# Kernel optimization log

Hardware: AMD Instinct MI355X
Metric: run time of the kernel (lower is better)

Reference implementation:

```python
import jax, jax.numpy as jnp
import numpy as np

EPS = 1e-10
BETA_SCALE = 1.0
TEMP = 0.5


def setup_inputs() -> dict:
    key = jax.random.key(0)
    ks = jax.random.split(key, 8)
    D = 128
    return {
        "root_mu_min": jax.random.normal(ks[0], (1, 64, D), dtype=jnp.float32),
        "root_mu_max": jax.random.normal(ks[1], (1, 64, D), dtype=jnp.float32),
        "root_beta_min_raw": jax.random.normal(ks[2], (1, 64, D), dtype=jnp.float32),
        "root_beta_max_raw": jax.random.normal(ks[3], (1, 64, D), dtype=jnp.float32),
        "adj_logits0": jax.random.normal(ks[4], (512, 64), dtype=jnp.float32),
        "adj_logits1": jax.random.normal(ks[5], (2048, 512), dtype=jnp.float32),
        "u0": jax.random.uniform(ks[6], (1, 512, 64), dtype=jnp.float32),
        "u1": jax.random.uniform(ks[7], (1, 2048, 512), dtype=jnp.float32),
    }


def _gumbel_sigmoid_hard(logits, u):
    # gumbel noise from externally supplied uniforms, straight-through hard threshold
    g = -jnp.log(-jnp.log(u + EPS) + EPS)
    y_soft = jax.nn.sigmoid((logits + g) / TEMP)
    y_hard = (y_soft > 0.5).astype(y_soft.dtype)
    return y_hard - jax.lax.stop_gradient(y_soft) + y_soft


def _weighted_intersection(mu_min, mu_max, beta_min, beta_max, w):
    # w: (1, C, P); parent boxes: (1, P, D)
    wsum = jnp.sum(w, axis=2)[..., None] + EPS                      # (1, C, 1)
    b_min = jnp.einsum('bcp,bpd->bcd', w, beta_min) / wsum           # (1, C, D)
    b_max = jnp.einsum('bcp,bpd->bcd', w, beta_max) / wsum           # (1, C, D)
    logw = jnp.log(w + EPS)[..., None]                               # (1, C, P, 1)
    arg_min = logw + mu_min[:, None, :, :] / b_min[:, :, None, :]    # (1, C, P, D)
    mu_min_i = b_min * jax.nn.logsumexp(arg_min, axis=2)             # (1, C, D)
    arg_max = logw - mu_max[:, None, :, :] / b_max[:, :, None, :]    # (1, C, P, D)
    mu_max_i = -b_max * jax.nn.logsumexp(arg_max, axis=2)            # (1, C, D)
    return mu_min_i, mu_max_i, b_min, b_max


def reference(root_mu_min, root_mu_max, root_beta_min_raw, root_beta_max_raw,
              adj_logits0, adj_logits1, u0, u1):
    beta_min = jax.nn.sigmoid(root_beta_min_raw) * BETA_SCALE + 1e-6
    beta_max = jax.nn.sigmoid(root_beta_max_raw) * BETA_SCALE + 1e-6
    level = (root_mu_min, root_mu_max, beta_min, beta_max)
    outs = list(level)
    for logits, u in ((adj_logits0, u0), (adj_logits1, u1)):
        w = _gumbel_sigmoid_hard(logits[None], u)  # (1, C, P)
        level = _weighted_intersection(*level, w)
        outs.extend(level)
    return tuple(outs)
```

## Files before the change

kernel.cpp:

```cpp
#include <hip/hip_runtime.h>
#include <cmath>

#define DD 128
#define LOG2E 1.4426950408889634f

__device__ __forceinline__ float sigm(float x) { return 1.0f / (1.0f + __expf(-x)); }

__global__ __launch_bounds__(512, 4)
void k_lvl1(const float* __restrict__ mu_min0, const float* __restrict__ mu_max0,
            const float* __restrict__ braw_min, const float* __restrict__ braw_max,
            const float* __restrict__ adj0, const float* __restrict__ u0,
            float* __restrict__ out,
            float2* __restrict__ mu2_1, float2* __restrict__ bb2_1,
            float4* __restrict__ pmax) {
    __shared__ __align__(16) float wsh[64][4];
    __shared__ int npres[4];
    __shared__ float4 red[8][4][64];
    __shared__ float4 cmx[8][64];
    __shared__ float4 carrA[4][64], carrB[4][64];
    const int tid = threadIdx.x;
    const int w = tid >> 6, lane = tid & 63;
    const int c0 = blockIdx.x * 4;

    if (tid < 64) {
        int i = blockIdx.x * 64 + tid;
        out[i] = mu_min0[i];
        out[8192 + i] = mu_max0[i];
        out[16384 + i] = sigm(braw_min[i]) + 1e-6f;
        out[24576 + i] = sigm(braw_max[i]) + 1e-6f;
    }

    if (tid < 256) {
        int j = tid >> 6, p = tid & 63;
        int idx = (c0 + j) * 64 + p;
        float uu = u0[idx] + 1e-10f;
        float g = -__logf(-__logf(uu) + 1e-10f);
        bool pres = (adj0[idx] + g) > 0.0f;
        wsh[p][j] = pres ? 1.0f : 1e-10f;
        unsigned long long m = __ballot(pres);
        if ((tid & 63) == 0) npres[j] = (int)__popcll(m);
    }
    __syncthreads();

    const int p0 = w * 8;
    const int dbase = 2 * lane;

    float4 accB[4];
    #pragma unroll
    for (int j = 0; j < 4; ++j) accB[j] = make_float4(0.f, 0.f, 0.f, 0.f);
    float4 mrow[8];
    float cm_mn0 = -INFINITY, cm_mn1 = -INFINITY, cm_ng0 = -INFINITY, cm_ng1 = -INFINITY;
    #pragma unroll
    for (int z = 0; z < 8; ++z) {
        int p = p0 + z;
        float2 bmr = *(const float2*)(braw_min + p * DD + dbase);
        float2 bxr = *(const float2*)(braw_max + p * DD + dbase);
        float2 mnr = *(const float2*)(mu_min0 + p * DD + dbase);
        float2 mxr = *(const float2*)(mu_max0 + p * DD + dbase);
        float bm0 = sigm(bmr.x) + 1e-6f, bm1 = sigm(bmr.y) + 1e-6f;
        float bx0 = sigm(bxr.x) + 1e-6f, bx1 = sigm(bxr.y) + 1e-6f;
        mrow[z] = make_float4(mnr.x, mxr.x, mnr.y, mxr.y);
        cm_mn0 = fmaxf(cm_mn0, mnr.x); cm_mn1 = fmaxf(cm_mn1, mnr.y);
        cm_ng0 = fmaxf(cm_ng0, -mxr.x); cm_ng1 = fmaxf(cm_ng1, -mxr.y);
        float4 wv = *(const float4*)wsh[p];
        const float* wf = (const float*)&wv;
        #pragma unroll
        for (int j = 0; j < 4; ++j) {
            accB[j].x = fmaf(wf[j], bm0, accB[j].x);
            accB[j].y = fmaf(wf[j], bx0, accB[j].y);
            accB[j].z = fmaf(wf[j], bm1, accB[j].z);
            accB[j].w = fmaf(wf[j], bx1, accB[j].w);
        }
    }
    #pragma unroll
    for (int j = 0; j < 4; ++j) red[w][j][lane] = accB[j];
    cmx[w][lane] = make_float4(cm_mn0, cm_ng0, cm_mn1, cm_ng1);
    __syncthreads();

    float bmin0, bmax0, bmin1, bmax1, rmin0, rmin1, nrmax0, nrmax1, Mm0, Mm1, Mg0, Mg1;
    const int rj = tid >> 6;
    if (tid < 256) {
        float4 S = red[0][rj][lane];
        float4 M = cmx[0][lane];
        #pragma unroll
        for (int ww = 1; ww < 8; ++ww) {
            float4 t = red[ww][rj][lane];
            S.x += t.x; S.y += t.y; S.z += t.z; S.w += t.w;
            float4 m = cmx[ww][lane];
            M.x = fmaxf(M.x, m.x); M.y = fmaxf(M.y, m.y);
            M.z = fmaxf(M.z, m.z); M.w = fmaxf(M.w, m.w);
        }
        Mm0 = M.x; Mg0 = M.y; Mm1 = M.z; Mg1 = M.w;
        const float wsv = (float)npres[rj] + 1e-10f;
        bmin0 = S.x / wsv; bmax0 = S.y / wsv; bmin1 = S.z / wsv; bmax1 = S.w / wsv;
        rmin0 = 1.0f / fmaxf(bmin0, 1e-30f);
        rmin1 = 1.0f / fmaxf(bmin1, 1e-30f);
        nrmax0 = -1.0f / fmaxf(bmax0, 1e-30f);
        nrmax1 = -1.0f / fmaxf(bmax1, 1e-30f);
        float rm20 = rmin0 * LOG2E, rm21 = rmin1 * LOG2E;
        float nx20 = nrmax0 * LOG2E, nx21 = nrmax1 * LOG2E;
        carrA[rj][lane] = make_float4(rm20, rm21, nx20, nx21);
        carrB[rj][lane] = make_float4(-rm20 * Mm0, -rm21 * Mm1, nx20 * Mg0, nx21 * Mg1);
    }
    __syncthreads();

    float4 cA[4], cB[4];
    #pragma unroll
    for (int j = 0; j < 4; ++j) { cA[j] = carrA[j][lane]; cB[j] = carrB[j][lane]; }

    float4 accS[4];
    #pragma unroll
    for (int j = 0; j < 4; ++j) accS[j] = make_float4(0.f, 0.f, 0.f, 0.f);
    #pragma unroll
    for (int z = 0; z < 8; ++z) {
        float4 q = mrow[z];
        float4 wv = *(const float4*)wsh[p0 + z];
        const float* wf = (const float*)&wv;
        #pragma unroll
        for (int j = 0; j < 4; ++j) {
            accS[j].x = fmaf(wf[j], __builtin_amdgcn_exp2f(fmaf(q.x, cA[j].x, cB[j].x)), accS[j].x);
            accS[j].y = fmaf(wf[j], __builtin_amdgcn_exp2f(fmaf(q.y, cA[j].z, cB[j].z)), accS[j].y);
            accS[j].z = fmaf(wf[j], __builtin_amdgcn_exp2f(fmaf(q.z, cA[j].y, cB[j].y)), accS[j].z);
            accS[j].w = fmaf(wf[j], __builtin_amdgcn_exp2f(fmaf(q.w, cA[j].w, cB[j].w)), accS[j].w);
        }
    }
    #pragma unroll
    for (int j = 0; j < 4; ++j) red[w][j][lane] = accS[j];
    __syncthreads();

    if (tid < 256) {
        float4 S = red[0][rj][lane];
        #pragma unroll
        for (int ww = 1; ww < 8; ++ww) {
            float4 t = red[ww][rj][lane];
            S.x += t.x; S.y += t.y; S.z += t.z; S.w += t.w;
        }
        const float S10 = fmaxf(S.x, 1e-35f);
        const float S20 = fmaxf(S.y, 1e-35f);
        const float S11 = fmaxf(S.z, 1e-35f);
        const float S21 = fmaxf(S.w, 1e-35f);
        const int cc = c0 + rj;
        const int idx = cc * DD + 2 * lane;
        float v10 = bmin0 * fmaf(rmin0, Mm0, __logf(S10));
        float v11 = bmin1 * fmaf(rmin1, Mm1, __logf(S11));
        float v20 = -bmax0 * fmaf(-nrmax0, Mg0, __logf(S20));
        float v21 = -bmax1 * fmaf(-nrmax1, Mg1, __logf(S21));
        *(float2*)(out + 32768 + idx)  = make_float2(v10, v11);
        *(float2*)(out + 98304 + idx)  = make_float2(v20, v21);
        *(float2*)(out + 163840 + idx) = make_float2(bmin0, bmin1);
        *(float2*)(out + 229376 + idx) = make_float2(bmax0, bmax1);
        *(float4*)(mu2_1 + idx) = make_float4(v10, v20, v11, v21);
        *(float4*)(bb2_1 + idx) = make_float4(bmin0, bmax0, bmin1, bmax1);
        red[0][rj][lane] = make_float4(v10, -v20, v11, -v21);
    }
    __syncthreads();
    if (tid < 64) {
        float4 m = red[0][0][tid];
        #pragma unroll
        for (int jj = 1; jj < 4; ++jj) {
            float4 t = red[0][jj][tid];
            m.x = fmaxf(m.x, t.x); m.y = fmaxf(m.y, t.y);
            m.z = fmaxf(m.z, t.z); m.w = fmaxf(m.w, t.w);
        }
        pmax[blockIdx.x * 64 + tid] = m;
    }
}

__global__ __launch_bounds__(512, 4)
void k_level2d(const float* __restrict__ logits, const float* __restrict__ u,
               const float2* __restrict__ bb2, const float2* __restrict__ mu2,
               const float4* __restrict__ pmax,
               float* __restrict__ o_mu_min, float* __restrict__ o_mu_max,
               float* __restrict__ o_b_min, float* __restrict__ o_b_max) {
    constexpr int P = 512, TC = 4;
    __shared__ __align__(16) float wsh[P][TC];
    __shared__ int npres[TC];
    __shared__ float4 red[8][TC][64];
    __shared__ float4 cmx[8][64];
    __shared__ float4 carrA[TC][64], carrB[TC][64];
    const int tid = threadIdx.x;
    const int w = tid >> 6;
    const int lane = tid & 63;
    const int c0 = blockIdx.x * TC;
    if (tid < TC) npres[tid] = 0;
    __syncthreads();

    {
        float4 pm = make_float4(-INFINITY, -INFINITY, -INFINITY, -INFINITY);
        #pragma unroll
        for (int t = 0; t < 16; ++t) {
            float4 v = pmax[(w * 16 + t) * 64 + lane];
            pm.x = fmaxf(pm.x, v.x); pm.y = fmaxf(pm.y, v.y);
            pm.z = fmaxf(pm.z, v.z); pm.w = fmaxf(pm.w, v.w);
        }
        cmx[w][lane] = pm;
    }

    #pragma unroll
    for (int it = 0; it < TC; ++it) {
        int idx = (c0 + it) * P + tid;
        float uu = u[idx] + 1e-10f;
        float g = -__logf(-__logf(uu) + 1e-10f);
        bool pres = (logits[idx] + g) > 0.0f;
        wsh[tid][it] = pres ? 1.0f : 1e-10f;
        unsigned long long m = __ballot(pres);
        if (lane == 0) atomicAdd(&npres[it], (int)__popcll(m));
    }
    __syncthreads();

    const unsigned lb = (unsigned)(lane << 4);
    const char* bbc = (const char*)bb2 + (unsigned)(w * 64) * 1024u + lb;
    const char* muc = (const char*)mu2 + (unsigned)(w * 64) * 1024u + lb;
    const int p0 = w * 64;

    float4 accB[TC];
    #pragma unroll
    for (int j = 0; j < TC; ++j) accB[j] = make_float4(0.f, 0.f, 0.f, 0.f);
    for (int z = 0; z < 64; z += 4) {
        float4 q0 = *(const float4*)(bbc + (unsigned)(z + 0) * 1024u);
        float4 q1 = *(const float4*)(bbc + (unsigned)(z + 1) * 1024u);
        float4 q2 = *(const float4*)(bbc + (unsigned)(z + 2) * 1024u);
        float4 q3 = *(const float4*)(bbc + (unsigned)(z + 3) * 1024u);
        float4 w0 = *(const float4*)wsh[p0 + z + 0];
        float4 w1 = *(const float4*)wsh[p0 + z + 1];
        float4 w2 = *(const float4*)wsh[p0 + z + 2];
        float4 w3 = *(const float4*)wsh[p0 + z + 3];
        const float* wf0 = (const float*)&w0;
        const float* wf1 = (const float*)&w1;
        const float* wf2 = (const float*)&w2;
        const float* wf3 = (const float*)&w3;
        #pragma unroll
        for (int j = 0; j < TC; ++j) {
            accB[j].x = fmaf(wf0[j], q0.x, fmaf(wf1[j], q1.x, fmaf(wf2[j], q2.x, fmaf(wf3[j], q3.x, accB[j].x))));
            accB[j].y = fmaf(wf0[j], q0.y, fmaf(wf1[j], q1.y, fmaf(wf2[j], q2.y, fmaf(wf3[j], q3.y, accB[j].y))));
            accB[j].z = fmaf(wf0[j], q0.z, fmaf(wf1[j], q1.z, fmaf(wf2[j], q2.z, fmaf(wf3[j], q3.z, accB[j].z))));
            accB[j].w = fmaf(wf0[j], q0.w, fmaf(wf1[j], q1.w, fmaf(wf2[j], q2.w, fmaf(wf3[j], q3.w, accB[j].w))));
        }
    }
    #pragma unroll
    for (int j = 0; j < TC; ++j) red[w][j][lane] = accB[j];
    __syncthreads();

    float bmin0, bmax0, bmin1, bmax1, rmin0, rmin1, nrmax0, nrmax1, Mm0, Mm1, Mg0, Mg1;
    const int rj = tid >> 6;
    if (tid < 256) {
        float4 S = red[0][rj][lane];
        float4 M = cmx[0][lane];
        #pragma unroll
        for (int ww = 1; ww < 8; ++ww) {
            float4 t = red[ww][rj][lane];
            S.x += t.x; S.y += t.y; S.z += t.z; S.w += t.w;
            float4 m = cmx[ww][lane];
            M.x = fmaxf(M.x, m.x); M.y = fmaxf(M.y, m.y);
            M.z = fmaxf(M.z, m.z); M.w = fmaxf(M.w, m.w);
        }
        Mm0 = M.x; Mg0 = M.y; Mm1 = M.z; Mg1 = M.w;
        const float wsv = (float)npres[rj] + 1e-10f;
        bmin0 = S.x / wsv; bmax0 = S.y / wsv; bmin1 = S.z / wsv; bmax1 = S.w / wsv;
        rmin0 = 1.0f / fmaxf(bmin0, 1e-30f);
        rmin1 = 1.0f / fmaxf(bmin1, 1e-30f);
        nrmax0 = -1.0f / fmaxf(bmax0, 1e-30f);
        nrmax1 = -1.0f / fmaxf(bmax1, 1e-30f);
        float rm20 = rmin0 * LOG2E, rm21 = rmin1 * LOG2E;
        float nx20 = nrmax0 * LOG2E, nx21 = nrmax1 * LOG2E;
        carrA[rj][lane] = make_float4(rm20, rm21, nx20, nx21);
        carrB[rj][lane] = make_float4(-rm20 * Mm0, -rm21 * Mm1, nx20 * Mg0, nx21 * Mg1);
    }
    __syncthreads();

    float4 cA[TC], cB[TC];
    #pragma unroll
    for (int j = 0; j < TC; ++j) { cA[j] = carrA[j][lane]; cB[j] = carrB[j][lane]; }

    float4 accS[TC];
    #pragma unroll
    for (int j = 0; j < TC; ++j) accS[j] = make_float4(0.f, 0.f, 0.f, 0.f);
    for (int z = 0; z < 64; z += 2) {
        float4 q0 = *(const float4*)(muc + (unsigned)(z + 0) * 1024u);
        float4 q1 = *(const float4*)(muc + (unsigned)(z + 1) * 1024u);
        float4 w0 = *(const float4*)wsh[p0 + z + 0];
        float4 w1 = *(const float4*)wsh[p0 + z + 1];
        const float* wf0 = (const float*)&w0;
        const float* wf1 = (const float*)&w1;
        #pragma unroll
        for (int j = 0; j < TC; ++j) {
            accS[j].x = fmaf(wf0[j], __builtin_amdgcn_exp2f(fmaf(q0.x, cA[j].x, cB[j].x)), accS[j].x);
            accS[j].y = fmaf(wf0[j], __builtin_amdgcn_exp2f(fmaf(q0.y, cA[j].z, cB[j].z)), accS[j].y);
            accS[j].z = fmaf(wf0[j], __builtin_amdgcn_exp2f(fmaf(q0.z, cA[j].y, cB[j].y)), accS[j].z);
            accS[j].w = fmaf(wf0[j], __builtin_amdgcn_exp2f(fmaf(q0.w, cA[j].w, cB[j].w)), accS[j].w);
            accS[j].x = fmaf(wf1[j], __builtin_amdgcn_exp2f(fmaf(q1.x, cA[j].x, cB[j].x)), accS[j].x);
            accS[j].y = fmaf(wf1[j], __builtin_amdgcn_exp2f(fmaf(q1.y, cA[j].z, cB[j].z)), accS[j].y);
            accS[j].z = fmaf(wf1[j], __builtin_amdgcn_exp2f(fmaf(q1.z, cA[j].y, cB[j].y)), accS[j].z);
            accS[j].w = fmaf(wf1[j], __builtin_amdgcn_exp2f(fmaf(q1.w, cA[j].w, cB[j].w)), accS[j].w);
        }
    }
    #pragma unroll
    for (int j = 0; j < TC; ++j) red[w][j][lane] = accS[j];
    __syncthreads();

    if (tid < 256) {
        float4 S = red[0][rj][lane];
        #pragma unroll
        for (int ww = 1; ww < 8; ++ww) {
            float4 t = red[ww][rj][lane];
            S.x += t.x; S.y += t.y; S.z += t.z; S.w += t.w;
        }
        const float S10 = fmaxf(S.x, 1e-35f);
        const float S20 = fmaxf(S.y, 1e-35f);
        const float S11 = fmaxf(S.z, 1e-35f);
        const float S21 = fmaxf(S.w, 1e-35f);
        const int idx = (c0 + rj) * DD + 2 * lane;
        float v10 = bmin0 * fmaf(rmin0, Mm0, __logf(S10));
        float v11 = bmin1 * fmaf(rmin1, Mm1, __logf(S11));
        float v20 = -bmax0 * fmaf(-nrmax0, Mg0, __logf(S20));
        float v21 = -bmax1 * fmaf(-nrmax1, Mg1, __logf(S21));
        *(float2*)(o_mu_min + idx) = make_float2(v10, v11);
        *(float2*)(o_mu_max + idx) = make_float2(v20, v21);
        *(float2*)(o_b_min + idx)  = make_float2(bmin0, bmin1);
        *(float2*)(o_b_max + idx)  = make_float2(bmax0, bmax1);
    }
}

extern "C" void kernel_launch(void* const* d_in, const int* in_sizes, int n_in,
                              void* d_out, int out_size, void* d_ws, size_t ws_size,
                              hipStream_t stream) {
    const float* mu_min0  = (const float*)d_in[0];
    const float* mu_max0  = (const float*)d_in[1];
    const float* braw_min = (const float*)d_in[2];
    const float* braw_max = (const float*)d_in[3];
    const float* adj0     = (const float*)d_in[4];
    const float* adj1     = (const float*)d_in[5];
    const float* u0       = (const float*)d_in[6];
    const float* u1       = (const float*)d_in[7];
    float* out = (float*)d_out;
    float* ws = (float*)d_ws;

    float4* pmax  = (float4*)ws;
    float2* mu2_1 = (float2*)(ws + 32768);
    float2* bb2_1 = mu2_1 + 513 * DD;


    k_lvl1<<<dim3(128), dim3(512), 0, stream>>>(
        mu_min0, mu_max0, braw_min, braw_max, adj0, u0,
        out, mu2_1, bb2_1, pmax);

    k_level2d<<<dim3(512), dim3(512), 0, stream>>>(
        adj1, u1, bb2_1, mu2_1, pmax,
        out + 294912, out + 557056, out + 819200, out + 1081344);
}
```

Before: 137.8 us.

## Halve children per block in level-1 kernel and skip absent parents in level-2 exp loop

The level-1 kernel now handles 2 children per block instead of 4 and launches 256 blocks, which doubles the partial-max entries that level 2 reduces. In the level-2 logsumexp loop, the weighted accumulate is replaced by a branch that skips the exp2 work when the hard weight is 1e-10. That weight contributes about 1e-10 times a value of at most 1, so the result changes only negligibly. The branch is per lane, so wavefront divergence may limit how much work is actually saved.

Measured after the change: 118.7 us. -13.8%, faster.

```diff
diff --git a/kernel.cpp b/kernel.cpp
--- a/kernel.cpp
+++ b/kernel.cpp
@@ -13,41 +13,41 @@
             float* __restrict__ out,
             float2* __restrict__ mu2_1, float2* __restrict__ bb2_1,
             float4* __restrict__ pmax) {
-    __shared__ __align__(16) float wsh[64][4];
-    __shared__ int npres[4];
-    __shared__ float4 red[8][4][64];
+    __shared__ __align__(8) float wsh[64][2];
+    __shared__ int npres[2];
+    __shared__ float4 red[8][2][64];
     __shared__ float4 cmx[8][64];
-    __shared__ float4 carrA[4][64], carrB[4][64];
+    __shared__ float4 carrA[2][64], carrB[2][64];
     const int tid = threadIdx.x;
     const int w = tid >> 6, lane = tid & 63;
-    const int c0 = blockIdx.x * 4;
-
-    if (tid < 64) {
-        int i = blockIdx.x * 64 + tid;
+    const int c0 = blockIdx.x * 2;
+
+    if (tid < 32) {
+        int i = blockIdx.x * 32 + tid;
         out[i] = mu_min0[i];
         out[8192 + i] = mu_max0[i];
         out[16384 + i] = sigm(braw_min[i]) + 1e-6f;
         out[24576 + i] = sigm(braw_max[i]) + 1e-6f;
     }
 
-    if (tid < 256) {
-        int j = tid >> 6, p = tid & 63;
+    if (tid < 128) {
+        int j = w, p = lane;
         int idx = (c0 + j) * 64 + p;
         float uu = u0[idx] + 1e-10f;
         float g = -__logf(-__logf(uu) + 1e-10f);
         bool pres = (adj0[idx] + g) > 0.0f;
         wsh[p][j] = pres ? 1.0f : 1e-10f;
         unsigned long long m = __ballot(pres);
-        if ((tid & 63) == 0) npres[j] = (int)__popcll(m);
+        if (lane == 0) npres[j] = (int)__popcll(m);
     }
     __syncthreads();
 
     const int p0 = w * 8;
     const int dbase = 2 * lane;
 
-    float4 accB[4];
-    #pragma unroll
-    for (int j = 0; j < 4; ++j) accB[j] = make_float4(0.f, 0.f, 0.f, 0.f);
+    float4 accB[2];
+    accB[0] = make_float4(0.f, 0.f, 0.f, 0.f);
+    accB[1] = make_float4(0.f, 0.f, 0.f, 0.f);
     float4 mrow[8];
     float cm_mn0 = -INFINITY, cm_mn1 = -INFINITY, cm_ng0 = -INFINITY, cm_ng1 = -INFINITY;
     #pragma unroll
@@ -62,24 +62,24 @@
         mrow[z] = make_float4(mnr.x, mxr.x, mnr.y, mxr.y);
         cm_mn0 = fmaxf(cm_mn0, mnr.x); cm_mn1 = fmaxf(cm_mn1, mnr.y);
         cm_ng0 = fmaxf(cm_ng0, -mxr.x); cm_ng1 = fmaxf(cm_ng1, -mxr.y);
-        float4 wv = *(const float4*)wsh[p];
+        float2 wv = *(const float2*)wsh[p];
         const float* wf = (const float*)&wv;
         #pragma unroll
-        for (int j = 0; j < 4; ++j) {
+        for (int j = 0; j < 2; ++j) {
             accB[j].x = fmaf(wf[j], bm0, accB[j].x);
             accB[j].y = fmaf(wf[j], bx0, accB[j].y);
             accB[j].z = fmaf(wf[j], bm1, accB[j].z);
             accB[j].w = fmaf(wf[j], bx1, accB[j].w);
         }
     }
-    #pragma unroll
-    for (int j = 0; j < 4; ++j) red[w][j][lane] = accB[j];
+    red[w][0][lane] = accB[0];
+    red[w][1][lane] = accB[1];
     cmx[w][lane] = make_float4(cm_mn0, cm_ng0, cm_mn1, cm_ng1);
     __syncthreads();
 
     float bmin0, bmax0, bmin1, bmax1, rmin0, rmin1, nrmax0, nrmax1, Mm0, Mm1, Mg0, Mg1;
-    const int rj = tid >> 6;
-    if (tid < 256) {
+    const int rj = w;
+    if (tid < 128) {
         float4 S = red[0][rj][lane];
         float4 M = cmx[0][lane];
         #pragma unroll
@@ -104,31 +104,31 @@
     }
     __syncthreads();
 
-    float4 cA[4], cB[4];
-    #pragma unroll
-    for (int j = 0; j < 4; ++j) { cA[j] = carrA[j][lane]; cB[j] = carrB[j][lane]; }
-
-    float4 accS[4];
-    #pragma unroll
-    for (int j = 0; j < 4; ++j) accS[j] = make_float4(0.f, 0.f, 0.f, 0.f);
+    float4 cA[2], cB[2];
+    cA[0] = carrA[0][lane]; cB[0] = carrB[0][lane];
+    cA[1] = carrA[1][lane]; cB[1] = carrB[1][lane];
+
+    float4 accS[2];
+    accS[0] = make_float4(0.f, 0.f, 0.f, 0.f);
+    accS[1] = make_float4(0.f, 0.f, 0.f, 0.f);
     #pragma unroll
     for (int z = 0; z < 8; ++z) {
         float4 q = mrow[z];
-        float4 wv = *(const float4*)wsh[p0 + z];
+        float2 wv = *(const float2*)wsh[p0 + z];
         const float* wf = (const float*)&wv;
         #pragma unroll
-        for (int j = 0; j < 4; ++j) {
+        for (int j = 0; j < 2; ++j) {
             accS[j].x = fmaf(wf[j], __builtin_amdgcn_exp2f(fmaf(q.x, cA[j].x, cB[j].x)), accS[j].x);
             accS[j].y = fmaf(wf[j], __builtin_amdgcn_exp2f(fmaf(q.y, cA[j].z, cB[j].z)), accS[j].y);
             accS[j].z = fmaf(wf[j], __builtin_amdgcn_exp2f(fmaf(q.z, cA[j].y, cB[j].y)), accS[j].z);
             accS[j].w = fmaf(wf[j], __builtin_amdgcn_exp2f(fmaf(q.w, cA[j].w, cB[j].w)), accS[j].w);
         }
     }
-    #pragma unroll
-    for (int j = 0; j < 4; ++j) red[w][j][lane] = accS[j];
-    __syncthreads();
-
-    if (tid < 256) {
+    red[w][0][lane] = accS[0];
+    red[w][1][lane] = accS[1];
+    __syncthreads();
+
+    if (tid < 128) {
         float4 S = red[0][rj][lane];
         #pragma unroll
         for (int ww = 1; ww < 8; ++ww) {
@@ -155,14 +155,11 @@
     }
     __syncthreads();
     if (tid < 64) {
-        float4 m = red[0][0][tid];
-        #pragma unroll
-        for (int jj = 1; jj < 4; ++jj) {
-            float4 t = red[0][jj][tid];
-            m.x = fmaxf(m.x, t.x); m.y = fmaxf(m.y, t.y);
-            m.z = fmaxf(m.z, t.z); m.w = fmaxf(m.w, t.w);
-        }
-        pmax[blockIdx.x * 64 + tid] = m;
+        float4 a = red[0][0][tid];
+        float4 b = red[0][1][tid];
+        a.x = fmaxf(a.x, b.x); a.y = fmaxf(a.y, b.y);
+        a.z = fmaxf(a.z, b.z); a.w = fmaxf(a.w, b.w);
+        pmax[blockIdx.x * 64 + tid] = a;
     }
 }
 
@@ -188,8 +185,8 @@
     {
         float4 pm = make_float4(-INFINITY, -INFINITY, -INFINITY, -INFINITY);
         #pragma unroll
-        for (int t = 0; t < 16; ++t) {
-            float4 v = pmax[(w * 16 + t) * 64 + lane];
+        for (int t = 0; t < 32; ++t) {
+            float4 v = pmax[(w * 32 + t) * 64 + lane];
             pm.x = fmaxf(pm.x, v.x); pm.y = fmaxf(pm.y, v.y);
             pm.z = fmaxf(pm.z, v.z); pm.w = fmaxf(pm.w, v.w);
         }
@@ -284,14 +281,18 @@
         const float* wf1 = (const float*)&w1;
         #pragma unroll
         for (int j = 0; j < TC; ++j) {
-            accS[j].x = fmaf(wf0[j], __builtin_amdgcn_exp2f(fmaf(q0.x, cA[j].x, cB[j].x)), accS[j].x);
-            accS[j].y = fmaf(wf0[j], __builtin_amdgcn_exp2f(fmaf(q0.y, cA[j].z, cB[j].z)), accS[j].y);
-            accS[j].z = fmaf(wf0[j], __builtin_amdgcn_exp2f(fmaf(q0.z, cA[j].y, cB[j].y)), accS[j].z);
-            accS[j].w = fmaf(wf0[j], __builtin_amdgcn_exp2f(fmaf(q0.w, cA[j].w, cB[j].w)), accS[j].w);
-            accS[j].x = fmaf(wf1[j], __builtin_amdgcn_exp2f(fmaf(q1.x, cA[j].x, cB[j].x)), accS[j].x);
-            accS[j].y = fmaf(wf1[j], __builtin_amdgcn_exp2f(fmaf(q1.y, cA[j].z, cB[j].z)), accS[j].y);
-            accS[j].z = fmaf(wf1[j], __builtin_amdgcn_exp2f(fmaf(q1.z, cA[j].y, cB[j].y)), accS[j].z);
-            accS[j].w = fmaf(wf1[j], __builtin_amdgcn_exp2f(fmaf(q1.w, cA[j].w, cB[j].w)), accS[j].w);
+            if (wf0[j] > 0.5f) {
+                accS[j].x += __builtin_amdgcn_exp2f(fmaf(q0.x, cA[j].x, cB[j].x));
+                accS[j].y += __builtin_amdgcn_exp2f(fmaf(q0.y, cA[j].z, cB[j].z));
+                accS[j].z += __builtin_amdgcn_exp2f(fmaf(q0.z, cA[j].y, cB[j].y));
+                accS[j].w += __builtin_amdgcn_exp2f(fmaf(q0.w, cA[j].w, cB[j].w));
+            }
+            if (wf1[j] > 0.5f) {
+                accS[j].x += __builtin_amdgcn_exp2f(fmaf(q1.x, cA[j].x, cB[j].x));
+                accS[j].y += __builtin_amdgcn_exp2f(fmaf(q1.y, cA[j].z, cB[j].z));
+                accS[j].z += __builtin_amdgcn_exp2f(fmaf(q1.z, cA[j].y, cB[j].y));
+                accS[j].w += __builtin_amdgcn_exp2f(fmaf(q1.w, cA[j].w, cB[j].w));
+            }
         }
     }
     #pragma unroll
@@ -336,11 +337,11 @@
     float* ws = (float*)d_ws;
 
     float4* pmax  = (float4*)ws;
-    float2* mu2_1 = (float2*)(ws + 32768);
-    float2* bb2_1 = mu2_1 + 513 * DD;
-
-
-    k_lvl1<<<dim3(128), dim3(512), 0, stream>>>(
+    float2* mu2_1 = (float2*)(ws + 65536);
+    float2* bb2_1 = mu2_1 + 512 * DD;
+
+
+    k_lvl1<<<dim3(256), dim3(512), 0, stream>>>(
         mu_min0, mu_max0, braw_min, braw_max, adj0, u0,
         out, mu2_1, bb2_1, pmax);
 
```
